# Optimization experiments

Measured on AMD Instinct MI355X. Metric: run time of the kernel, lower is better.

The kernel has to match this reference:

```python
import jax, jax.numpy as jnp
import numpy as np

B, L, H, NH, DH = 2, 4096, 768, 12, 64
W_ = 128          # one-sided sliding window
NL = 2            # encoder layers
VOCAB, OUT, FF = 50265, 384, 3072
EPS = 1e-5


def _ln(x, s, b):
    m = jnp.mean(x, axis=-1, keepdims=True)
    v = jnp.mean((x - m) ** 2, axis=-1, keepdims=True)
    return (x - m) / jnp.sqrt(v + EPS) * s + b


def _attn(x, amask, Wq, bq, Wk, bk, Wv, bv, Wo, bo):
    # x: [B,L,H]; sliding-window attention (one-sided W_) + global token 0
    def heads(Wt, bt):
        return (x @ Wt + bt).reshape(B, L, NH, DH).transpose(0, 2, 1, 3)  # [B,NH,L,DH]
    q, k, v = heads(Wq, bq), heads(Wk, bk), heads(Wv, bv)
    scale = 1.0 / np.sqrt(DH).astype(np.float32)
    C = W_
    nC = L // C
    qc = q.reshape(B, NH, nC, C, DH)

    def blocks(t):  # gather [prev, self, next] key chunks -> [B,NH,nC,3C,DH]
        tc = t.reshape(B, NH, nC, C, DH)
        tp = jnp.pad(tc, ((0, 0), (0, 0), (1, 1), (0, 0), (0, 0)))
        return jnp.concatenate([tp[:, :, :-2], tp[:, :, 1:-1], tp[:, :, 2:]], axis=3)

    k3, v3 = blocks(k), blocks(v)
    s_loc = jnp.einsum('bhncd,bhnkd->bhnck', qc, k3) * scale  # [B,NH,nC,C,3C]

    pos_k = (jnp.arange(nC)[:, None] - 1) * C + jnp.arange(3 * C)[None, :]  # [nC,3C]
    pos_q = jnp.arange(nC)[:, None] * C + jnp.arange(C)[None, :]            # [nC,C]
    within = jnp.abs(pos_q[:, :, None] - pos_k[:, None, :]) <= W_           # [nC,C,3C]
    valid = (pos_k >= 0) & (pos_k < L) & (pos_k != 0)  # key 0 handled as global column
    mk = amask[:, jnp.clip(pos_k, 0, L - 1)] > 0        # [B,nC,3C]
    m = within[None, None] & valid[None, None, :, None, :] & mk[:, None, :, None, :]
    s_loc = jnp.where(m, s_loc, -1e9)

    # every token also attends to the global token 0
    s_g = jnp.einsum('bhld,bhd->bhl', q, k[:, :, 0]) * scale  # [B,NH,L]
    s = jnp.concatenate([s_loc.reshape(B, NH, L, 3 * C), s_g[..., None]], axis=-1)
    p = jax.nn.softmax(s, axis=-1)
    p_loc = p[..., :3 * C].reshape(B, NH, nC, C, 3 * C)
    out = jnp.einsum('bhnck,bhnkd->bhncd', p_loc, v3).reshape(B, NH, L, DH)
    out = out + p[..., -1:] * v[:, :, 0][:, :, None, :]

    # global token 0 attends to everything
    s0 = jnp.einsum('bhd,bhld->bhl', q[:, :, 0], k) * scale
    s0 = jnp.where(amask[:, None, :] > 0, s0, -1e9)
    o0 = jnp.einsum('bhl,bhld->bhd', jax.nn.softmax(s0, axis=-1), v)
    out = out.at[:, :, 0, :].set(o0)

    out = out.transpose(0, 2, 1, 3).reshape(B, L, H)
    return out @ Wo + bo


def setup_inputs() -> dict:
    key = jax.random.key(0)
    ks = jax.random.split(key, 16)
    p = lambda k_, sh: 0.02 * jax.random.normal(k_, sh, jnp.float32)
    return {
        'input_ids': jax.random.randint(ks[0], (B, L), 0, VOCAB, dtype=jnp.int32),
        'attention_mask': jnp.ones((B, L), jnp.int32),
        'word_emb': p(ks[1], (VOCAB, H)),
        'pos_emb': p(ks[2], (L, H)),
        'emb_ln_s': jnp.ones((H,), jnp.float32), 'emb_ln_b': jnp.zeros((H,), jnp.float32),
        'Wq': p(ks[3], (NL, H, H)), 'bq': jnp.zeros((NL, H), jnp.float32),
        'Wk': p(ks[4], (NL, H, H)), 'bk': jnp.zeros((NL, H), jnp.float32),
        'Wv': p(ks[5], (NL, H, H)), 'bv': jnp.zeros((NL, H), jnp.float32),
        'Wo': p(ks[6], (NL, H, H)), 'bo': jnp.zeros((NL, H), jnp.float32),
        'ln1_s': jnp.ones((NL, H), jnp.float32), 'ln1_b': jnp.zeros((NL, H), jnp.float32),
        'W1': p(ks[7], (NL, H, FF)), 'b1': jnp.zeros((NL, FF), jnp.float32),
        'W2': p(ks[8], (NL, FF, H)), 'b2': jnp.zeros((NL, H), jnp.float32),
        'ln2_s': jnp.ones((NL, H), jnp.float32), 'ln2_b': jnp.zeros((NL, H), jnp.float32),
        'Wfc': p(ks[9], (H, OUT)), 'bfc': jnp.zeros((OUT,), jnp.float32),
    }


def reference(input_ids, attention_mask, word_emb, pos_emb, emb_ln_s, emb_ln_b,
              Wq, bq, Wk, bk, Wv, bv, Wo, bo, ln1_s, ln1_b,
              W1, b1, W2, b2, ln2_s, ln2_b, Wfc, bfc):
    x = word_emb[input_ids] + pos_emb[None]
    x = _ln(x, emb_ln_s, emb_ln_b)
    for l in range(NL):
        a = _attn(x, attention_mask, Wq[l], bq[l], Wk[l], bk[l], Wv[l], bv[l], Wo[l], bo[l])
        x = _ln(x + a, ln1_s[l], ln1_b[l])
        h = jax.nn.gelu(x @ W1[l] + b1[l])
        x = _ln(x + h @ W2[l] + b2[l], ln2_s[l], ln2_b[l])
    v_dn = x @ Wfc + bfc           # [B,L,OUT]
    cls = v_dn[:, 0]               # fc(last_hidden[:,0]) == v_dn[:,0]
    return v_dn, cls
```

## Files before the change

### kernel.cpp

```cpp
#include <hip/hip_runtime.h>
#include <hip/hip_bf16.h>
#include <stdint.h>

#define L_SEQ 4096
#define H_DIM 768
#define N_HEADS 12
#define D_HEAD 64
#define N_CHUNK 32
#define CHUNK 128
#define FF_DIM 3072
#define OUT_DIM 384
#define BATCH 2
#define EPS_LN 1e-5f
#define M_ROWS (BATCH * L_SEQ)
#define QKV_LD (3 * H_DIM)
#define NSEG 16

typedef unsigned short u16;
typedef __bf16 bx8 __attribute__((ext_vector_type(8)));
typedef float fx4 __attribute__((ext_vector_type(4)));
typedef u16 ux8 __attribute__((ext_vector_type(8)));

__device__ __forceinline__ u16 f2bf(float f) {
  union { float f; unsigned u; } x; x.f = f;
  unsigned r = x.u + 0x7fffu + ((x.u >> 16) & 1u);
  return (u16)(r >> 16);
}
__device__ __forceinline__ float bf2f(u16 v) {
  union { unsigned u; float f; } x; x.u = ((unsigned)v) << 16;
  return x.f;
}

__device__ __forceinline__ void gload16(const void* g, void* l) {
  __builtin_amdgcn_global_load_lds((const __attribute__((address_space(1))) void*)g,
                                   (__attribute__((address_space(3))) void*)l, 16, 0, 0);
}

template<int OUT_BF16, int DO_GELU, int DO_CLS>
__global__ __launch_bounds__(256, 3)
void gemm_s(const u16* __restrict__ A, const u16* __restrict__ Bt,
            const float* __restrict__ bias,
            float* __restrict__ Cf, u16* __restrict__ Cb,
            float* __restrict__ cls,
            int N, int K)
{
  __shared__ __align__(16) u16 As[128 * 64];
  __shared__ __align__(16) u16 Bs[128 * 64];
  const int tid = threadIdx.x;
  const int lane = tid & 63, w = tid >> 6;
  const int c16 = lane & 15, g = lane >> 4;
  const int wr = w >> 1, wc = w & 1;

  const int nbn = N >> 7;
  int id = blockIdx.x;
  id = (id & 7) * (gridDim.x >> 3) + (id >> 3);
  const int bm = id / nbn, bn = id % nbn;

  const int srow = w * 8 + (lane >> 3);
  const int schunk = (lane & 7) ^ (lane >> 3);
  const u16* sA = A + (size_t)(bm * 128 + srow) * K + schunk * 8;
  const u16* sB = Bt + (size_t)(bn * 128 + srow) * K + schunk * 8;
  const int wdst = w * 512;

  fx4 acc[4][4] = {};

  for (int k0 = 0; k0 < K; k0 += 64) {
    #pragma unroll
    for (int i = 0; i < 4; i++) {
      gload16(sA + (size_t)(i * 32) * K + k0, &As[i * 2048 + wdst]);
      gload16(sB + (size_t)(i * 32) * K + k0, &Bs[i * 2048 + wdst]);
    }
    __syncthreads();
    #pragma unroll
    for (int h = 0; h < 2; h++) {
      bx8 af[4], bf[4];
      #pragma unroll
      for (int m = 0; m < 4; m++) {
        const int row = wr * 64 + m * 16 + c16;
        af[m] = *(const bx8*)&As[row * 64 + (((h << 2) + g) ^ (c16 & 7)) * 8];
      }
      #pragma unroll
      for (int n = 0; n < 4; n++) {
        const int row = wc * 64 + n * 16 + c16;
        bf[n] = *(const bx8*)&Bs[row * 64 + (((h << 2) + g) ^ (c16 & 7)) * 8];
      }
      #pragma unroll
      for (int m = 0; m < 4; m++)
        #pragma unroll
        for (int n = 0; n < 4; n++)
          acc[m][n] = __builtin_amdgcn_mfma_f32_16x16x32_bf16(af[m], bf[n], acc[m][n], 0, 0, 0);
    }
    __syncthreads();
  }

  const int row0 = bm * 128 + wr * 64 + g * 4;
  const int col0 = bn * 128 + wc * 64 + c16;
  #pragma unroll
  for (int n = 0; n < 4; n++) {
    const int col = col0 + n * 16;
    const float bb = bias[col];
    #pragma unroll
    for (int m = 0; m < 4; m++) {
      #pragma unroll
      for (int r = 0; r < 4; r++) {
        float y = acc[m][n][r] + bb;
        if (DO_GELU) {
          const float tt = y;
          y = 0.5f * tt * (1.0f + tanhf(0.7978845608f * (tt + 0.044715f * tt * tt * tt)));
        }
        const int row = row0 + m * 16 + r;
        const size_t idx = (size_t)row * N + col;
        if (OUT_BF16) Cb[idx] = f2bf(y);
        else Cf[idx] = y;
        if (DO_CLS) {
          if ((row & (L_SEQ - 1)) == 0)
            cls[(row >> 12) * OUT_DIM + col] = y;
        }
      }
    }
  }
}

#define P2_STR 64

__global__ __launch_bounds__(512, 2)
void attn_local_kernel(const u16* __restrict__ qkv, const int* __restrict__ amask,
                       u16* __restrict__ attnout)
{
  __shared__ __align__(16) u16 Klds[2][64 * 64];
  __shared__ __align__(16) u16 Vlds[2][64 * 64];
  __shared__ __align__(16) u16 Plds[8 * 16 * P2_STR];

  const int tid = threadIdx.x;
  const int lane = tid & 63, w = tid >> 6;
  const int c16 = lane & 15, g = lane >> 4;

  const int bh = blockIdx.x >> 5;
  const int n = blockIdx.x & 31;
  const int b = bh / N_HEADS, h = bh % N_HEADS;

  const u16* qkvb = qkv + (size_t)b * L_SEQ * QKV_LD + h * D_HEAD;
  const int chunk_lo = n * CHUNK - CHUNK;

  const int qrow = n * CHUNK + w * 16 + c16;
  const u16* qp = qkvb + (size_t)qrow * QKV_LD + g * 8;
  const bx8 aq0 = *(const bx8*)qp;
  const bx8 aq1 = *(const bx8*)(qp + 32);

  unsigned kvm = 0;
  #pragma unroll
  for (int kf = 0; kf < 24; kf++) {
    const int pos = chunk_lo + kf * 16 + c16;
    bool ok = (pos >= 1) && (pos < L_SEQ);
    if (ok) ok = (amask[b * L_SEQ + pos] > 0);
    kvm |= ((unsigned)ok) << kf;
  }

  const int cq = w * 16 + g * 4;

  float m[4], l[4], pgv[4];
  {
    const u16* kp = qkvb + H_DIM + g * 8;
    const bx8 b0 = *(const bx8*)kp;
    const bx8 b1 = *(const bx8*)(kp + 32);
    fx4 sg = {};
    sg = __builtin_amdgcn_mfma_f32_16x16x32_bf16(aq0, b0, sg, 0, 0, 0);
    sg = __builtin_amdgcn_mfma_f32_16x16x32_bf16(aq1, b1, sg, 0, 0, 0);
    #pragma unroll
    for (int r = 0; r < 4; r++) {
      const float val = (c16 == 0) ? sg[r] * 0.125f : -1.0e9f;
      float mm = val;
      mm = fmaxf(mm, __shfl_xor(mm, 1));
      mm = fmaxf(mm, __shfl_xor(mm, 2));
      mm = fmaxf(mm, __shfl_xor(mm, 4));
      mm = fmaxf(mm, __shfl_xor(mm, 8));
      m[r] = mm;
      pgv[r] = __expf(val - mm);
      float t = pgv[r];
      t += __shfl_xor(t, 1);
      t += __shfl_xor(t, 2);
      t += __shfl_xor(t, 4);
      t += __shfl_xor(t, 8);
      l[r] = t;
    }
  }

  const int krow_s = w * 8 + (lane >> 3);
  const int ksc = (lane & 7) ^ (krow_s & 7);
  const int d = lane;
  const int vdst = d * 64 + ((w ^ (d & 7)) << 3);

  {
    int pos = chunk_lo + krow_s;
    if (pos < 0) pos = 0;
    if (pos >= L_SEQ) pos = L_SEQ - 1;
    gload16(qkvb + (size_t)pos * QKV_LD + H_DIM + ksc * 8, &Klds[0][w * 512]);
  }
  ux8 vreg;
  #pragma unroll
  for (int j = 0; j < 8; j++) {
    int pos = chunk_lo + w * 8 + j;
    if (pos < 0) pos = 0;
    if (pos >= L_SEQ) pos = L_SEQ - 1;
    vreg[j] = qkvb[(size_t)pos * QKV_LD + 2 * H_DIM + d];
  }
  *(ux8*)&Vlds[0][vdst] = vreg;
  __syncthreads();

  fx4 o[4] = {};
  u16* pb = Plds + w * 16 * P2_STR;
  const int prow = (w * 16 + c16) * P2_STR;

  for (int t = 0; t < 6; t++) {
    const int cur = t & 1, nxt = cur ^ 1;

    if (t < 5) {
      int pos = chunk_lo + (t + 1) * 64 + krow_s;
      if (pos < 0) pos = 0;
      if (pos >= L_SEQ) pos = L_SEQ - 1;
      gload16(qkvb + (size_t)pos * QKV_LD + H_DIM + ksc * 8, &Klds[nxt][w * 512]);
      #pragma unroll
      for (int j = 0; j < 8; j++) {
        int vp = chunk_lo + (t + 1) * 64 + w * 8 + j;
        if (vp < 0) vp = 0;
        if (vp >= L_SEQ) vp = L_SEQ - 1;
        vreg[j] = qkvb[(size_t)vp * QKV_LD + 2 * H_DIM + d];
      }
    }

    fx4 s[4];
    __builtin_amdgcn_s_setprio(1);
    #pragma unroll
    for (int kf = 0; kf < 4; kf++) {
      const int krow = kf * 16 + c16;
      const bx8 b0 = *(const bx8*)&Klds[cur][krow * 64 + ((g ^ (c16 & 7)) << 3)];
      const bx8 b1 = *(const bx8*)&Klds[cur][krow * 64 + (((4 + g) ^ (c16 & 7)) << 3)];
      fx4 a = {};
      a = __builtin_amdgcn_mfma_f32_16x16x32_bf16(aq0, b0, a, 0, 0, 0);
      a = __builtin_amdgcn_mfma_f32_16x16x32_bf16(aq1, b1, a, 0, 0, 0);
      s[kf] = a;
    }
    __builtin_amdgcn_s_setprio(0);
    float pmax[4];
    #pragma unroll
    for (int r = 0; r < 4; r++) pmax[r] = -3.0e38f;
    #pragma unroll
    for (int kf = 0; kf < 4; kf++) {
      const int KF = t * 4 + kf;
      const int j = KF * 16 + c16;
      const bool kv = ((kvm >> KF) & 1u) != 0;
      #pragma unroll
      for (int r = 0; r < 4; r++) {
        const int c = cq + r;
        const bool keep = kv && (j >= c && j <= c + 256);
        const float val = keep ? s[kf][r] * 0.125f : -1.0e9f;
        s[kf][r] = val;
        pmax[r] = fmaxf(pmax[r], val);
      }
    }
    #pragma unroll
    for (int r = 0; r < 4; r++) {
      float mm = pmax[r];
      mm = fmaxf(mm, __shfl_xor(mm, 1));
      mm = fmaxf(mm, __shfl_xor(mm, 2));
      mm = fmaxf(mm, __shfl_xor(mm, 4));
      mm = fmaxf(mm, __shfl_xor(mm, 8));
      const float newm = fmaxf(m[r], mm);
      const float scale = __expf(m[r] - newm);
      m[r] = newm;
      l[r] *= scale;
      pgv[r] *= scale;
      #pragma unroll
      for (int df = 0; df < 4; df++) o[df][r] *= scale;
    }
    float lsum[4] = {0.f, 0.f, 0.f, 0.f};
    #pragma unroll
    for (int kf = 0; kf < 4; kf++)
      #pragma unroll
      for (int r = 0; r < 4; r++) {
        const float p = __expf(s[kf][r] - m[r]);
        s[kf][r] = p;
        lsum[r] += p;
      }
    #pragma unroll
    for (int r = 0; r < 4; r++) {
      float tt = lsum[r];
      tt += __shfl_xor(tt, 1);
      tt += __shfl_xor(tt, 2);
      tt += __shfl_xor(tt, 4);
      tt += __shfl_xor(tt, 8);
      l[r] += tt;
    }
    #pragma unroll
    for (int kf = 0; kf < 4; kf++) {
      #pragma unroll
      for (int r = 0; r < 4; r++) {
        const int rr = g * 4 + r;
        const int jj = kf * 16 + c16;
        pb[rr * P2_STR + (((jj >> 3) ^ (rr & 7)) << 3) + (jj & 7)] = f2bf(s[kf][r]);
      }
    }
    __builtin_amdgcn_s_setprio(1);
    #pragma unroll
    for (int kt = 0; kt < 2; kt++) {
      const int ckp = kt * 4 + g;
      const bx8 pa = *(const bx8*)&Plds[prow + ((ckp ^ (c16 & 7)) << 3)];
      #pragma unroll
      for (int df = 0; df < 4; df++) {
        const int vrow = df * 16 + c16;
        const bx8 vvf = *(const bx8*)&Vlds[cur][vrow * 64 + ((ckp ^ (c16 & 7)) << 3)];
        o[df] = __builtin_amdgcn_mfma_f32_16x16x32_bf16(pa, vvf, o[df], 0, 0, 0);
      }
    }
    __builtin_amdgcn_s_setprio(0);
    if (t < 5) *(ux8*)&Vlds[nxt][vdst] = vreg;
    __syncthreads();
  }

  float rinv[4], pg[4];
  #pragma unroll
  for (int r = 0; r < 4; r++) {
    rinv[r] = 1.0f / l[r];
    pg[r] = __shfl(pgv[r], g * 16);
  }
  u16* ob = attnout + (size_t)b * L_SEQ * H_DIM + h * D_HEAD;
  const int posq = n * CHUNK + w * 16 + g * 4;
  #pragma unroll
  for (int df = 0; df < 4; df++) {
    const float v0f = bf2f(qkvb[2 * H_DIM + df * 16 + c16]);
    #pragma unroll
    for (int r = 0; r < 4; r++)
      ob[(size_t)(posq + r) * H_DIM + df * 16 + c16] =
          f2bf((o[df][r] + pg[r] * v0f) * rinv[r]);
  }
}

__global__ __launch_bounds__(256)
void attn_g_score(const u16* __restrict__ qkv, const int* __restrict__ amask,
                  float* __restrict__ sbuf, float* __restrict__ pmax)
{
  __shared__ float qs[D_HEAD];
  __shared__ float red[4];
  const int seg = blockIdx.x, bh = blockIdx.y;
  const int b = bh / N_HEADS, h = bh % N_HEADS;
  const u16* base = qkv + (size_t)b * L_SEQ * QKV_LD + h * D_HEAD;
  const int tid = threadIdx.x;

  if (tid < D_HEAD) qs[tid] = bf2f(base[tid]);
  __syncthreads();

  const int l = seg * 256 + tid;
  const ux8* kp = (const ux8*)(base + (size_t)l * QKV_LD + H_DIM);
  float dot = 0.f;
  #pragma unroll
  for (int i = 0; i < 8; i++) {
    const ux8 kv = kp[i];
    #pragma unroll
    for (int j = 0; j < 8; j++) dot += qs[i * 8 + j] * bf2f(kv[j]);
  }
  float sv = dot * 0.125f;
  if (amask[b * L_SEQ + l] == 0) sv = -1.0e9f;
  sbuf[(size_t)bh * L_SEQ + l] = sv;

  float m = sv;
  #pragma unroll
  for (int off = 32; off > 0; off >>= 1) m = fmaxf(m, __shfl_xor(m, off));
  if ((tid & 63) == 0) red[tid >> 6] = m;
  __syncthreads();
  if (tid == 0)
    pmax[bh * NSEG + seg] = fmaxf(fmaxf(red[0], red[1]), fmaxf(red[2], red[3]));
}

__global__ __launch_bounds__(256)
void attn_g_pv(const u16* __restrict__ qkv, const float* __restrict__ sbuf,
               const float* __restrict__ pmax, float* __restrict__ psum,
               float* __restrict__ po)
{
  __shared__ float es[256];
  __shared__ float red[4];
  const int seg = blockIdx.x, bh = blockIdx.y;
  const int b = bh / N_HEADS, h = bh % N_HEADS;
  const int tid = threadIdx.x;

  float M = -3.0e38f;
  #pragma unroll
  for (int i = 0; i < NSEG; i++) M = fmaxf(M, pmax[bh * NSEG + i]);

  const int l = seg * 256 + tid;
  const float e = __expf(sbuf[(size_t)bh * L_SEQ + l] - M);
  es[tid] = e;

  float t = e;
  #pragma unroll
  for (int off = 32; off > 0; off >>= 1) t += __shfl_xor(t, off);
  if ((tid & 63) == 0) red[tid >> 6] = t;
  __syncthreads();
  if (tid == 0) psum[bh * NSEG + seg] = red[0] + red[1] + red[2] + red[3];

  const int d = tid & 63, grp = tid >> 6;
  const u16* vb = qkv + (size_t)b * L_SEQ * QKV_LD + h * D_HEAD + 2 * H_DIM + d;
  float acc = 0.f;
  #pragma unroll 4
  for (int i = 0; i < 64; i++) {
    const int ll = seg * 256 + grp * 64 + i;
    acc += es[grp * 64 + i] * bf2f(vb[(size_t)ll * QKV_LD]);
  }
  po[(((size_t)bh * NSEG + seg) * 4 + grp) * D_HEAD + d] = acc;
}

__global__ __launch_bounds__(64)
void attn_g_combine(const float* __restrict__ psum, const float* __restrict__ po,
                    u16* __restrict__ attnout)
{
  const int bh = blockIdx.x;
  const int b = bh / N_HEADS, h = bh % N_HEADS;
  const int d = threadIdx.x;
  float S = 0.f;
  #pragma unroll
  for (int i = 0; i < NSEG; i++) S += psum[bh * NSEG + i];
  float acc = 0.f;
  #pragma unroll
  for (int i = 0; i < NSEG * 4; i++)
    acc += po[((size_t)bh * NSEG * 4 + i) * D_HEAD + d];
  attnout[(size_t)b * L_SEQ * H_DIM + h * D_HEAD + d] = f2bf(acc / S);
}

__device__ __forceinline__ void block_stats(float sum, float sq, float* red,
                                            float& mean, float& rstd)
{
  const int lane = threadIdx.x & 63, wv = threadIdx.x >> 6;
  #pragma unroll
  for (int off = 32; off > 0; off >>= 1) {
    sum += __shfl_xor(sum, off);
    sq  += __shfl_xor(sq, off);
  }
  if (lane == 0) { red[wv] = sum; red[4 + wv] = sq; }
  __syncthreads();
  sum = red[0] + red[1] + red[2] + red[3];
  sq  = red[4] + red[5] + red[6] + red[7];
  mean = sum * (1.0f / H_DIM);
  const float var = sq * (1.0f / H_DIM) - mean * mean;
  rstd = rsqrtf(var + EPS_LN);
}

__global__ __launch_bounds__(256)
void embed_ln_kernel(const int* __restrict__ ids, const float* __restrict__ wemb,
                     const float* __restrict__ pemb, const float* __restrict__ gam,
                     const float* __restrict__ bet, u16* __restrict__ xb)
{
  __shared__ float red[8];
  const int row = blockIdx.x, tid = threadIdx.x;
  const int l = row & (L_SEQ - 1);
  const int id = ids[row];
  float v[3]; float sum = 0.f, sq = 0.f;
  #pragma unroll
  for (int i = 0; i < 3; i++) {
    const int c = tid + i * 256;
    const float t = wemb[(size_t)id * H_DIM + c] + pemb[(size_t)l * H_DIM + c];
    v[i] = t; sum += t; sq += t * t;
  }
  float mean, rstd;
  block_stats(sum, sq, red, mean, rstd);
  #pragma unroll
  for (int i = 0; i < 3; i++) {
    const int c = tid + i * 256;
    const float y = (v[i] - mean) * rstd * gam[c] + bet[c];
    xb[(size_t)row * H_DIM + c] = f2bf(y);
  }
}

__global__ __launch_bounds__(256)
void add_ln_kernel(u16* xio, const u16* __restrict__ yin,
                   const float* __restrict__ gam, const float* __restrict__ bet)
{
  __shared__ float red[8];
  const int row = blockIdx.x, tid = threadIdx.x;
  float v[3]; float sum = 0.f, sq = 0.f;
  #pragma unroll
  for (int i = 0; i < 3; i++) {
    const int c = tid + i * 256;
    const float t = bf2f(xio[(size_t)row * H_DIM + c]) + bf2f(yin[(size_t)row * H_DIM + c]);
    v[i] = t; sum += t; sq += t * t;
  }
  float mean, rstd;
  block_stats(sum, sq, red, mean, rstd);
  #pragma unroll
  for (int i = 0; i < 3; i++) {
    const int c = tid + i * 256;
    const float y = (v[i] - mean) * rstd * gam[c] + bet[c];
    xio[(size_t)row * H_DIM + c] = f2bf(y);
  }
}

__global__ __launch_bounds__(256)
void prep_weights(const float* __restrict__ Wq, const float* __restrict__ Wk,
                  const float* __restrict__ Wv, const float* __restrict__ Wo,
                  const float* __restrict__ W1, const float* __restrict__ W2,
                  const float* __restrict__ Wfc,
                  const float* __restrict__ bq, const float* __restrict__ bk,
                  const float* __restrict__ bv,
                  u16* __restrict__ wqkvT, u16* __restrict__ woT,
                  u16* __restrict__ w1T, u16* __restrict__ w2T,
                  u16* __restrict__ wfcT, float* __restrict__ bqkv)
{
  const int t = blockIdx.x;
  const int tid = threadIdx.x;
  if (t >= 14112) {
    const int idx = t - 14112;
    const int l = idx / 9, j = idx % 9;
    const int i = j * 256 + tid;
    if (i < H_DIM)          bqkv[l * QKV_LD + i] = bq[l * H_DIM + i];
    else if (i < 2 * H_DIM) bqkv[l * QKV_LD + i] = bk[l * H_DIM + i - H_DIM];
    else if (i < 3 * H_DIM) bqkv[l * QKV_LD + i] = bv[l * H_DIM + i - 2 * H_DIM];
    return;
  }
  const float* src; u16* dst; int K, N, r;
  if (t < 13824) {
    const int l = t / 6912; r = t % 6912;
    if (r < 2304) {
      const int m = r / 576; r = r % 576; K = H_DIM; N = H_DIM;
      if (m == 0)      src = Wq + (size_t)l * H_DIM * H_DIM;
      else if (m == 1) src = Wk + (size_t)l * H_DIM * H_DIM;
      else if (m == 2) src = Wv + (size_t)l * H_DIM * H_DIM;
      else             src = Wo + (size_t)l * H_DIM * H_DIM;
      dst = (m < 3) ? wqkvT + (size_t)l * QKV_LD * H_DIM + (size_t)m * H_DIM * H_DIM
                    : woT + (size_t)l * H_DIM * H_DIM;
    } else if (r < 4608) {
      r -= 2304; K = H_DIM; N = FF_DIM;
      src = W1 + (size_t)l * H_DIM * FF_DIM;
      dst = w1T + (size_t)l * FF_DIM * H_DIM;
    } else {
      r -= 4608; K = FF_DIM; N = H_DIM;
      src = W2 + (size_t)l * FF_DIM * H_DIM;
      dst = w2T + (size_t)l * H_DIM * FF_DIM;
    }
  } else {
    r = t - 13824; K = H_DIM; N = OUT_DIM; src = Wfc; dst = wfcT;
  }
  const int ntn = N >> 5;
  const int k0 = (r / ntn) * 32, n0 = (r % ntn) * 32;
  __shared__ float tile[32][33];
  const int tx = tid & 31, ty = tid >> 5;
  #pragma unroll
  for (int i = 0; i < 32; i += 8)
    tile[ty + i][tx] = src[(size_t)(k0 + ty + i) * N + n0 + tx];
  __syncthreads();
  #pragma unroll
  for (int i = 0; i < 32; i += 8)
    dst[(size_t)(n0 + ty + i) * K + k0 + tx] = f2bf(tile[tx][ty + i]);
}

extern "C" void kernel_launch(void* const* d_in, const int* in_sizes, int n_in,
                              void* d_out, int out_size, void* d_ws, size_t ws_size,
                              hipStream_t stream)
{
  (void)in_sizes; (void)n_in; (void)out_size; (void)ws_size;
  const int*   ids   = (const int*)d_in[0];
  const int*   amask = (const int*)d_in[1];
  const float* wemb  = (const float*)d_in[2];
  const float* pemb  = (const float*)d_in[3];
  const float* elns  = (const float*)d_in[4];
  const float* elnb  = (const float*)d_in[5];
  const float* Wq    = (const float*)d_in[6];
  const float* bq    = (const float*)d_in[7];
  const float* Wk    = (const float*)d_in[8];
  const float* bk    = (const float*)d_in[9];
  const float* Wv    = (const float*)d_in[10];
  const float* bv    = (const float*)d_in[11];
  const float* Wo    = (const float*)d_in[12];
  const float* bo    = (const float*)d_in[13];
  const float* ln1s  = (const float*)d_in[14];
  const float* ln1b  = (const float*)d_in[15];
  const float* W1    = (const float*)d_in[16];
  const float* b1    = (const float*)d_in[17];
  const float* W2    = (const float*)d_in[18];
  const float* b2    = (const float*)d_in[19];
  const float* ln2s  = (const float*)d_in[20];
  const float* ln2b  = (const float*)d_in[21];
  const float* Wfc   = (const float*)d_in[22];
  const float* bfc   = (const float*)d_in[23];

  char* ws = (char*)d_ws;
  size_t off = 0;
  auto alloc = [&](size_t bytes) -> void* {
    void* p = ws + off;
    off += (bytes + 255) & ~(size_t)255;
    return p;
  };
  u16* xb     = (u16*)alloc((size_t)M_ROWS * H_DIM * 2);
  u16* projb  = (u16*)alloc((size_t)M_ROWS * H_DIM * 2);
  u16* big    = (u16*)alloc((size_t)M_ROWS * FF_DIM * 2);
  u16* attno  = (u16*)alloc((size_t)M_ROWS * H_DIM * 2);
  u16* wqkvT  = (u16*)alloc((size_t)2 * QKV_LD * H_DIM * 2);
  u16* woT    = (u16*)alloc((size_t)2 * H_DIM * H_DIM * 2);
  u16* w1T    = (u16*)alloc((size_t)2 * FF_DIM * H_DIM * 2);
  u16* w2T    = (u16*)alloc((size_t)2 * H_DIM * FF_DIM * 2);
  u16* wfcT   = (u16*)alloc((size_t)OUT_DIM * H_DIM * 2);
  float* bqkv = (float*)alloc(2 * QKV_LD * 4);
  float* gsc  = (float*)alloc((size_t)BATCH * N_HEADS * L_SEQ * 4);
  float* gpm  = (float*)alloc((size_t)BATCH * N_HEADS * NSEG * 4);
  float* gps  = (float*)alloc((size_t)BATCH * N_HEADS * NSEG * 4);
  float* gpo  = (float*)alloc((size_t)BATCH * N_HEADS * NSEG * 4 * D_HEAD * 4);

  u16* qkvb = big;
  u16* ff1  = big;

  prep_weights<<<14130, 256, 0, stream>>>(Wq, Wk, Wv, Wo, W1, W2, Wfc,
                                          bq, bk, bv,
                                          wqkvT, woT, w1T, w2T, wfcT, bqkv);
  embed_ln_kernel<<<M_ROWS, 256, 0, stream>>>(ids, wemb, pemb, elns, elnb, xb);

  for (int l = 0; l < 2; l++) {
    gemm_s<1, 0, 0><<<(M_ROWS / 128) * (QKV_LD / 128), 256, 0, stream>>>(
        xb, wqkvT + (size_t)l * QKV_LD * H_DIM, bqkv + l * QKV_LD,
        nullptr, qkvb, nullptr, QKV_LD, H_DIM);
    attn_local_kernel<<<BATCH * N_HEADS * N_CHUNK, 512, 0, stream>>>(qkvb, amask, attno);
    attn_g_score<<<dim3(NSEG, BATCH * N_HEADS), 256, 0, stream>>>(qkvb, amask, gsc, gpm);
    attn_g_pv<<<dim3(NSEG, BATCH * N_HEADS), 256, 0, stream>>>(qkvb, gsc, gpm, gps, gpo);
    attn_g_combine<<<BATCH * N_HEADS, 64, 0, stream>>>(gps, gpo, attno);
    gemm_s<1, 0, 0><<<(M_ROWS / 128) * (H_DIM / 128), 256, 0, stream>>>(
        attno, woT + (size_t)l * H_DIM * H_DIM, bo + l * H_DIM,
        nullptr, projb, nullptr, H_DIM, H_DIM);
    add_ln_kernel<<<M_ROWS, 256, 0, stream>>>(xb, projb, ln1s + l * H_DIM, ln1b + l * H_DIM);
    gemm_s<1, 1, 0><<<(M_ROWS / 128) * (FF_DIM / 128), 256, 0, stream>>>(
        xb, w1T + (size_t)l * FF_DIM * H_DIM, b1 + l * FF_DIM,
        nullptr, ff1, nullptr, FF_DIM, H_DIM);
    gemm_s<1, 0, 0><<<(M_ROWS / 128) * (H_DIM / 128), 256, 0, stream>>>(
        ff1, w2T + (size_t)l * H_DIM * FF_DIM, b2 + l * H_DIM,
        nullptr, projb, nullptr, H_DIM, FF_DIM);
    add_ln_kernel<<<M_ROWS, 256, 0, stream>>>(xb, projb, ln2s + l * H_DIM, ln2b + l * H_DIM);
  }

  float* vdn = (float*)d_out;
  float* cls = vdn + (size_t)BATCH * L_SEQ * OUT_DIM;
  gemm_s<0, 0, 1><<<(M_ROWS / 128) * (OUT_DIM / 128), 256, 0, stream>>>(
      xb, wfcT, bfc, vdn, nullptr, cls, OUT_DIM, H_DIM);
}
```

Baseline: 557.5 us.

## Fuse global-token attention into local attention kernel and merge embed into prep

Global-token-0 attention now runs as extra blocks inside the local attention kernel, each computing scores, a local max, exp sums and partial PV over 512 keys. A rescaling combine step merges these partials with per-segment maxima, so the separate score and PV kernels and the fp32 score buffer are gone. The embedding LayerNorm is also folded into the weight-prep kernel as extra blocks, so both run in one launch. This cuts two kernel launches per layer plus one at setup, at the cost of branchy heterogeneous blocks that share the local kernel's 512-thread launch bounds and LDS.

```diff
diff --git a/kernel.cpp b/kernel.cpp
--- a/kernel.cpp
+++ b/kernel.cpp
@@ -14,7 +14,8 @@
 #define EPS_LN 1e-5f
 #define M_ROWS (BATCH * L_SEQ)
 #define QKV_LD (3 * H_DIM)
-#define NSEG 16
+#define NLOC (BATCH * N_HEADS * N_CHUNK)
+#define NGSEG 8
 
 typedef unsigned short u16;
 typedef __bf16 bx8 __attribute__((ext_vector_type(8)));
@@ -124,8 +125,10 @@
 #define P2_STR 64
 
 __global__ __launch_bounds__(512, 2)
-void attn_local_kernel(const u16* __restrict__ qkv, const int* __restrict__ amask,
-                       u16* __restrict__ attnout)
+void attn_fused_kernel(const u16* __restrict__ qkv, const int* __restrict__ amask,
+                       u16* __restrict__ attnout,
+                       float* __restrict__ gpm, float* __restrict__ gps,
+                       float* __restrict__ gpo)
 {
   __shared__ __align__(16) u16 Klds[2][64 * 64];
   __shared__ __align__(16) u16 Vlds[2][64 * 64];
@@ -133,8 +136,67 @@
 
   const int tid = threadIdx.x;
   const int lane = tid & 63, w = tid >> 6;
+
+  if (blockIdx.x >= NLOC) {
+    float* fsc = (float*)&Klds[0][0];
+    float* qs  = fsc;
+    float* es  = fsc + 64;
+    float* red = fsc + 576;
+    const int idx = blockIdx.x - NLOC;
+    const int bh = idx >> 3, seg = idx & 7;
+    const int b = bh / N_HEADS, h = bh % N_HEADS;
+    const u16* base = qkv + (size_t)b * L_SEQ * QKV_LD + h * D_HEAD;
+
+    if (tid < D_HEAD) qs[tid] = bf2f(base[tid]);
+    __syncthreads();
+
+    const int key = seg * 512 + tid;
+    const ux8* kp = (const ux8*)(base + (size_t)key * QKV_LD + H_DIM);
+    float dot = 0.f;
+    #pragma unroll
+    for (int i = 0; i < 8; i++) {
+      const ux8 kv = kp[i];
+      #pragma unroll
+      for (int j = 0; j < 8; j++) dot += qs[i * 8 + j] * bf2f(kv[j]);
+    }
+    float sv = dot * 0.125f;
+    if (amask[b * L_SEQ + key] == 0) sv = -1.0e9f;
+
+    float mv = sv;
+    #pragma unroll
+    for (int off = 32; off > 0; off >>= 1) mv = fmaxf(mv, __shfl_xor(mv, off));
+    if (lane == 0) red[w] = mv;
+    __syncthreads();
+    float M = -3.0e38f;
+    #pragma unroll
+    for (int i = 0; i < 8; i++) M = fmaxf(M, red[i]);
+
+    const float e = __expf(sv - M);
+    es[tid] = e;
+    float s = e;
+    #pragma unroll
+    for (int off = 32; off > 0; off >>= 1) s += __shfl_xor(s, off);
+    __syncthreads();
+    if (lane == 0) red[w] = s;
+    __syncthreads();
+    float Sl = 0.f;
+    #pragma unroll
+    for (int i = 0; i < 8; i++) Sl += red[i];
+
+    const int gi = tid >> 6, d = lane;
+    const u16* vb = base + 2 * H_DIM + d;
+    float acc = 0.f;
+    #pragma unroll 4
+    for (int i = 0; i < 64; i++) {
+      const int kk = seg * 512 + gi * 64 + i;
+      acc += es[gi * 64 + i] * bf2f(vb[(size_t)kk * QKV_LD]);
+    }
+    gpo[(((size_t)bh * NGSEG + seg) * 8 + gi) * D_HEAD + d] = acc;
+    if (tid == 0) { gpm[bh * NGSEG + seg] = M; gps[bh * NGSEG + seg] = Sl; }
+    return;
+  }
+
   const int c16 = lane & 15, g = lane >> 4;
-
   const int bh = blockIdx.x >> 5;
   const int n = blockIdx.x & 31;
   const int b = bh / N_HEADS, h = bh % N_HEADS;
@@ -335,93 +397,25 @@
   }
 }
 
-__global__ __launch_bounds__(256)
-void attn_g_score(const u16* __restrict__ qkv, const int* __restrict__ amask,
-                  float* __restrict__ sbuf, float* __restrict__ pmax)
-{
-  __shared__ float qs[D_HEAD];
-  __shared__ float red[4];
-  const int seg = blockIdx.x, bh = blockIdx.y;
-  const int b = bh / N_HEADS, h = bh % N_HEADS;
-  const u16* base = qkv + (size_t)b * L_SEQ * QKV_LD + h * D_HEAD;
-  const int tid = threadIdx.x;
-
-  if (tid < D_HEAD) qs[tid] = bf2f(base[tid]);
-  __syncthreads();
-
-  const int l = seg * 256 + tid;
-  const ux8* kp = (const ux8*)(base + (size_t)l * QKV_LD + H_DIM);
-  float dot = 0.f;
-  #pragma unroll
-  for (int i = 0; i < 8; i++) {
-    const ux8 kv = kp[i];
-    #pragma unroll
-    for (int j = 0; j < 8; j++) dot += qs[i * 8 + j] * bf2f(kv[j]);
-  }
-  float sv = dot * 0.125f;
-  if (amask[b * L_SEQ + l] == 0) sv = -1.0e9f;
-  sbuf[(size_t)bh * L_SEQ + l] = sv;
-
-  float m = sv;
-  #pragma unroll
-  for (int off = 32; off > 0; off >>= 1) m = fmaxf(m, __shfl_xor(m, off));
-  if ((tid & 63) == 0) red[tid >> 6] = m;
-  __syncthreads();
-  if (tid == 0)
-    pmax[bh * NSEG + seg] = fmaxf(fmaxf(red[0], red[1]), fmaxf(red[2], red[3]));
-}
-
-__global__ __launch_bounds__(256)
-void attn_g_pv(const u16* __restrict__ qkv, const float* __restrict__ sbuf,
-               const float* __restrict__ pmax, float* __restrict__ psum,
-               float* __restrict__ po)
-{
-  __shared__ float es[256];
-  __shared__ float red[4];
-  const int seg = blockIdx.x, bh = blockIdx.y;
-  const int b = bh / N_HEADS, h = bh % N_HEADS;
-  const int tid = threadIdx.x;
-
-  float M = -3.0e38f;
-  #pragma unroll
-  for (int i = 0; i < NSEG; i++) M = fmaxf(M, pmax[bh * NSEG + i]);
-
-  const int l = seg * 256 + tid;
-  const float e = __expf(sbuf[(size_t)bh * L_SEQ + l] - M);
-  es[tid] = e;
-
-  float t = e;
-  #pragma unroll
-  for (int off = 32; off > 0; off >>= 1) t += __shfl_xor(t, off);
-  if ((tid & 63) == 0) red[tid >> 6] = t;
-  __syncthreads();
-  if (tid == 0) psum[bh * NSEG + seg] = red[0] + red[1] + red[2] + red[3];
-
-  const int d = tid & 63, grp = tid >> 6;
-  const u16* vb = qkv + (size_t)b * L_SEQ * QKV_LD + h * D_HEAD + 2 * H_DIM + d;
-  float acc = 0.f;
-  #pragma unroll 4
-  for (int i = 0; i < 64; i++) {
-    const int ll = seg * 256 + grp * 64 + i;
-    acc += es[grp * 64 + i] * bf2f(vb[(size_t)ll * QKV_LD]);
-  }
-  po[(((size_t)bh * NSEG + seg) * 4 + grp) * D_HEAD + d] = acc;
-}
-
 __global__ __launch_bounds__(64)
-void attn_g_combine(const float* __restrict__ psum, const float* __restrict__ po,
-                    u16* __restrict__ attnout)
+void attn_g_combine(const float* __restrict__ gpm, const float* __restrict__ gps,
+                    const float* __restrict__ gpo, u16* __restrict__ attnout)
 {
   const int bh = blockIdx.x;
   const int b = bh / N_HEADS, h = bh % N_HEADS;
   const int d = threadIdx.x;
-  float S = 0.f;
-  #pragma unroll
-  for (int i = 0; i < NSEG; i++) S += psum[bh * NSEG + i];
-  float acc = 0.f;
-  #pragma unroll
-  for (int i = 0; i < NSEG * 4; i++)
-    acc += po[((size_t)bh * NSEG * 4 + i) * D_HEAD + d];
+  float M = -3.0e38f;
+  #pragma unroll
+  for (int s = 0; s < NGSEG; s++) M = fmaxf(M, gpm[bh * NGSEG + s]);
+  float S = 0.f, acc = 0.f;
+  #pragma unroll
+  for (int s = 0; s < NGSEG; s++) {
+    const float sc = __expf(gpm[bh * NGSEG + s] - M);
+    S += gps[bh * NGSEG + s] * sc;
+    #pragma unroll
+    for (int gi = 0; gi < 8; gi++)
+      acc += gpo[(((size_t)bh * NGSEG + s) * 8 + gi) * D_HEAD + d] * sc;
+  }
   attnout[(size_t)b * L_SEQ * H_DIM + h * D_HEAD + d] = f2bf(acc / S);
 }
 
@@ -444,32 +438,6 @@
 }
 
 __global__ __launch_bounds__(256)
-void embed_ln_kernel(const int* __restrict__ ids, const float* __restrict__ wemb,
-                     const float* __restrict__ pemb, const float* __restrict__ gam,
-                     const float* __restrict__ bet, u16* __restrict__ xb)
-{
-  __shared__ float red[8];
-  const int row = blockIdx.x, tid = threadIdx.x;
-  const int l = row & (L_SEQ - 1);
-  const int id = ids[row];
-  float v[3]; float sum = 0.f, sq = 0.f;
-  #pragma unroll
-  for (int i = 0; i < 3; i++) {
-    const int c = tid + i * 256;
-    const float t = wemb[(size_t)id * H_DIM + c] + pemb[(size_t)l * H_DIM + c];
-    v[i] = t; sum += t; sq += t * t;
-  }
-  float mean, rstd;
-  block_stats(sum, sq, red, mean, rstd);
-  #pragma unroll
-  for (int i = 0; i < 3; i++) {
-    const int c = tid + i * 256;
-    const float y = (v[i] - mean) * rstd * gam[c] + bet[c];
-    xb[(size_t)row * H_DIM + c] = f2bf(y);
-  }
-}
-
-__global__ __launch_bounds__(256)
 void add_ln_kernel(u16* xio, const u16* __restrict__ yin,
                    const float* __restrict__ gam, const float* __restrict__ bet)
 {
@@ -493,18 +461,44 @@
 }
 
 __global__ __launch_bounds__(256)
-void prep_weights(const float* __restrict__ Wq, const float* __restrict__ Wk,
-                  const float* __restrict__ Wv, const float* __restrict__ Wo,
-                  const float* __restrict__ W1, const float* __restrict__ W2,
-                  const float* __restrict__ Wfc,
-                  const float* __restrict__ bq, const float* __restrict__ bk,
-                  const float* __restrict__ bv,
-                  u16* __restrict__ wqkvT, u16* __restrict__ woT,
-                  u16* __restrict__ w1T, u16* __restrict__ w2T,
-                  u16* __restrict__ wfcT, float* __restrict__ bqkv)
+void prep_embed(const float* __restrict__ Wq, const float* __restrict__ Wk,
+                const float* __restrict__ Wv, const float* __restrict__ Wo,
+                const float* __restrict__ W1, const float* __restrict__ W2,
+                const float* __restrict__ Wfc,
+                const float* __restrict__ bq, const float* __restrict__ bk,
+                const float* __restrict__ bv,
+                u16* __restrict__ wqkvT, u16* __restrict__ woT,
+                u16* __restrict__ w1T, u16* __restrict__ w2T,
+                u16* __restrict__ wfcT, float* __restrict__ bqkv,
+                const int* __restrict__ ids, const float* __restrict__ wemb,
+                const float* __restrict__ pemb, const float* __restrict__ gam,
+                const float* __restrict__ bet, u16* __restrict__ xb)
 {
   const int t = blockIdx.x;
   const int tid = threadIdx.x;
+  __shared__ float tile[32][33];
+
+  if (t >= 14130) {
+    const int row = t - 14130;
+    const int l = row & (L_SEQ - 1);
+    const int id = ids[row];
+    float v[3]; float sum = 0.f, sq = 0.f;
+    #pragma unroll
+    for (int i = 0; i < 3; i++) {
+      const int c = tid + i * 256;
+      const float x = wemb[(size_t)id * H_DIM + c] + pemb[(size_t)l * H_DIM + c];
+      v[i] = x; sum += x; sq += x * x;
+    }
+    float mean, rstd;
+    block_stats(sum, sq, &tile[0][0], mean, rstd);
+    #pragma unroll
+    for (int i = 0; i < 3; i++) {
+      const int c = tid + i * 256;
+      const float y = (v[i] - mean) * rstd * gam[c] + bet[c];
+      xb[(size_t)row * H_DIM + c] = f2bf(y);
+    }
+    return;
+  }
   if (t >= 14112) {
     const int idx = t - 14112;
     const int l = idx / 9, j = idx % 9;
@@ -518,13 +512,13 @@
   if (t < 13824) {
     const int l = t / 6912; r = t % 6912;
     if (r < 2304) {
-      const int m = r / 576; r = r % 576; K = H_DIM; N = H_DIM;
-      if (m == 0)      src = Wq + (size_t)l * H_DIM * H_DIM;
-      else if (m == 1) src = Wk + (size_t)l * H_DIM * H_DIM;
-      else if (m == 2) src = Wv + (size_t)l * H_DIM * H_DIM;
-      else             src = Wo + (size_t)l * H_DIM * H_DIM;
-      dst = (m < 3) ? wqkvT + (size_t)l * QKV_LD * H_DIM + (size_t)m * H_DIM * H_DIM
-                    : woT + (size_t)l * H_DIM * H_DIM;
+      const int mq = r / 576; r = r % 576; K = H_DIM; N = H_DIM;
+      if (mq == 0)      src = Wq + (size_t)l * H_DIM * H_DIM;
+      else if (mq == 1) src = Wk + (size_t)l * H_DIM * H_DIM;
+      else if (mq == 2) src = Wv + (size_t)l * H_DIM * H_DIM;
+      else              src = Wo + (size_t)l * H_DIM * H_DIM;
+      dst = (mq < 3) ? wqkvT + (size_t)l * QKV_LD * H_DIM + (size_t)mq * H_DIM * H_DIM
+                     : woT + (size_t)l * H_DIM * H_DIM;
     } else if (r < 4608) {
       r -= 2304; K = H_DIM; N = FF_DIM;
       src = W1 + (size_t)l * H_DIM * FF_DIM;
@@ -539,7 +533,6 @@
   }
   const int ntn = N >> 5;
   const int k0 = (r / ntn) * 32, n0 = (r % ntn) * 32;
-  __shared__ float tile[32][33];
   const int tx = tid & 31, ty = tid >> 5;
   #pragma unroll
   for (int i = 0; i < 32; i += 8)
@@ -597,27 +590,25 @@
   u16* w2T    = (u16*)alloc((size_t)2 * H_DIM * FF_DIM * 2);
   u16* wfcT   = (u16*)alloc((size_t)OUT_DIM * H_DIM * 2);
   float* bqkv = (float*)alloc(2 * QKV_LD * 4);
-  float* gsc  = (float*)alloc((size_t)BATCH * N_HEADS * L_SEQ * 4);
-  float* gpm  = (float*)alloc((size_t)BATCH * N_HEADS * NSEG * 4);
-  float* gps  = (float*)alloc((size_t)BATCH * N_HEADS * NSEG * 4);
-  float* gpo  = (float*)alloc((size_t)BATCH * N_HEADS * NSEG * 4 * D_HEAD * 4);
+  float* gpm  = (float*)alloc((size_t)BATCH * N_HEADS * NGSEG * 4);
+  float* gps  = (float*)alloc((size_t)BATCH * N_HEADS * NGSEG * 4);
+  float* gpo  = (float*)alloc((size_t)BATCH * N_HEADS * NGSEG * 8 * D_HEAD * 4);
 
   u16* qkvb = big;
   u16* ff1  = big;
 
-  prep_weights<<<14130, 256, 0, stream>>>(Wq, Wk, Wv, Wo, W1, W2, Wfc,
-                                          bq, bk, bv,
-                                          wqkvT, woT, w1T, w2T, wfcT, bqkv);
-  embed_ln_kernel<<<M_ROWS, 256, 0, stream>>>(ids, wemb, pemb, elns, elnb, xb);
+  prep_embed<<<14130 + M_ROWS, 256, 0, stream>>>(
+      Wq, Wk, Wv, Wo, W1, W2, Wfc, bq, bk, bv,
+      wqkvT, woT, w1T, w2T, wfcT, bqkv,
+      ids, wemb, pemb, elns, elnb, xb);
 
   for (int l = 0; l < 2; l++) {
     gemm_s<1, 0, 0><<<(M_ROWS / 128) * (QKV_LD / 128), 256, 0, stream>>>(
         xb, wqkvT + (size_t)l * QKV_LD * H_DIM, bqkv + l * QKV_LD,
         nullptr, qkvb, nullptr, QKV_LD, H_DIM);
-    attn_local_kernel<<<BATCH * N_HEADS * N_CHUNK, 512, 0, stream>>>(qkvb, amask, attno);
-    attn_g_score<<<dim3(NSEG, BATCH * N_HEADS), 256, 0, stream>>>(qkvb, amask, gsc, gpm);
-    attn_g_pv<<<dim3(NSEG, BATCH * N_HEADS), 256, 0, stream>>>(qkvb, gsc, gpm, gps, gpo);
-    attn_g_combine<<<BATCH * N_HEADS, 64, 0, stream>>>(gps, gpo, attno);
+    attn_fused_kernel<<<NLOC + BATCH * N_HEADS * NGSEG, 512, 0, stream>>>(
+        qkvb, amask, attno, gpm, gps, gpo);
+    attn_g_combine<<<BATCH * N_HEADS, 64, 0, stream>>>(gpm, gps, gpo, attno);
     gemm_s<1, 0, 0><<<(M_ROWS / 128) * (H_DIM / 128), 256, 0, stream>>>(
         attno, woT + (size_t)l * H_DIM * H_DIM, bo + l * H_DIM,
         nullptr, projb, nullptr, H_DIM, H_DIM);
```

Result: slower. 591.8 us (+6.1%).
